# Kernel optimization log

Measured on AMD Instinct MI355X. Metric: run time of the kernel, lower is better.

Reference implementation:

```python
import jax, jax.numpy as jnp
import numpy as np
from jax import lax

DIM = 96
HEADS = 6
H = W = D = 64
EPS = 1e-12  # torch F.normalize default


def setup_inputs() -> dict:
    key = jax.random.key(0)
    k1, k2, k3, k4 = jax.random.split(key, 4)
    x = jax.random.normal(k1, (1, DIM, H, W, D), dtype=jnp.float32)
    # qkv 1x1 conv weight, stored as (3*dim, dim) matrix
    w_qkv = jax.random.normal(k2, (3 * DIM, DIM), dtype=jnp.float32) * (1.0 / np.sqrt(DIM))
    # depthwise 3x3x3 conv weight (OIDHW with I=1, groups=3*dim)
    w_dw = jax.random.normal(k3, (3 * DIM, 1, 3, 3, 3), dtype=jnp.float32) * (1.0 / np.sqrt(27))
    # output 1x1 conv weight as (dim, dim)
    w_proj = jax.random.normal(k4, (DIM, DIM), dtype=jnp.float32) * (1.0 / np.sqrt(DIM))
    temperature = jnp.ones((HEADS, 1, 1), dtype=jnp.float32)
    return {"x": x, "w_qkv": w_qkv, "w_dw": w_dw, "w_proj": w_proj, "temperature": temperature}


def _l2norm(t):
    # torch F.normalize(dim=-1): t / max(||t||, eps)
    n = jnp.sqrt(jnp.sum(t * t, axis=-1, keepdims=True))
    return t / jnp.maximum(n, EPS)


def reference(x, w_qkv, w_dw, w_proj, temperature):
    b, c, h, w, d = x.shape
    ch = c // HEADS  # per-head channels
    # 1x1 conv -> pointwise GEMM over channels
    qkv = jnp.einsum('bchwd,oc->bohwd', x, w_qkv)  # (b, 3c, h, w, d)
    # depthwise 3x3x3 conv, padding 1
    qkv = lax.conv_general_dilated(
        qkv, w_dw, window_strides=(1, 1, 1), padding=[(1, 1)] * 3,
        feature_group_count=3 * c,
        dimension_numbers=('NCDHW', 'OIDHW', 'NCDHW'))
    q, k, v = jnp.split(qkv, 3, axis=1)
    n = h * w * d
    q = q.reshape(b, HEADS, ch, n)
    k = k.reshape(b, HEADS, ch, n)
    v = v.reshape(b, HEADS, ch, n)
    q = _l2norm(q)
    k = _l2norm(k)
    # channel-wise attention: (b, heads, ch, ch)
    attn = jnp.einsum('bhcn,bhdn->bhcd', q, k) * temperature[None]
    attn = jax.nn.softmax(attn, axis=-1)
    out = jnp.einsum('bhcd,bhdn->bhcn', attn, v)  # (b, heads, ch, n)
    out = out.reshape(b, c, h, w, d)
    out = jnp.einsum('bchwd,oc->bohwd', out, w_proj)
    return out
```

## Files before the change

kernel.cpp:

```cpp
#include <hip/hip_runtime.h>
#include <hip/hip_bf16.h>
#include <hip/hip_fp16.h>

#define NTOT 262144
typedef __hip_bfloat16 bf16;
typedef __attribute__((ext_vector_type(4))) float f32x4;
typedef _Float16 f16x8 __attribute__((ext_vector_type(8)));

__device__ inline ushort f2bf(float f){ bf16 b = __float2bfloat16(f); return *(ushort*)&b; }
__device__ inline float bf2f(ushort u){ union{unsigned i;float f;}v; v.i = (unsigned)u<<16; return v.f; }
__device__ inline unsigned h2u(__half2 h){ union{__half2 h; unsigned u;}v; v.h=h; return v.u; }
__device__ inline __half2 u2h(unsigned u){ union{unsigned u; __half2 h;}v; v.u=u; return v.h; }
__device__ inline ushort f2h(float f){ __half h = __float2half_rn(f); return *(ushort*)&h; }

__global__ void detect_dtype(const ushort* __restrict__ w, int* __restrict__ flag) {
  int tid = threadIdx.x;
  int sane = 0;
  for (int i = tid; i < 512; i += 64) {
    ushort u = w[2 * i];
    int e = (u >> 7) & 0xff;
    sane += (e == 0 || (e >= 100 && e <= 140)) ? 1 : 0;
  }
#pragma unroll
  for (int off = 32; off > 0; off >>= 1) sane += __shfl_down(sane, off, 64);
  if (tid == 0) *flag = (sane >= 256) ? 1 : 0;
}

__global__ void cvt_f16(const void* __restrict__ in, ushort* __restrict__ outw,
                        int n, const int* __restrict__ flag) {
  int f = *flag;
  for (int i = blockIdx.x * 256 + threadIdx.x; i < n; i += gridDim.x * 256) {
    float v = f ? bf2f(((const ushort*)in)[i]) : ((const float*)in)[i];
    outw[i] = f2h(v);
  }
}

template<int MODE>
__global__ __launch_bounds__(256)
void transpose96(const void* __restrict__ in, ushort* __restrict__ out,
                 const int* __restrict__ flag) {
  __shared__ float t[96][65];
  const int tid = threadIdx.x;
  const long n0 = (long)blockIdx.x * 64;
  const int f = (MODE == 0) ? *flag : 0;
#pragma unroll
  for (int i = 0; i < 6; i++) {
    int idx = tid + 256 * i;
    int u = idx & 15, c = idx >> 4;
    float v0, v1, v2, v3;
    if (MODE == 0 && !f) {
      float4 q = *(const float4*)((const float*)in + (size_t)c * NTOT + n0 + u * 4);
      v0 = q.x; v1 = q.y; v2 = q.z; v3 = q.w;
    } else if (MODE == 0) {
      uint2 q = *(const uint2*)((const ushort*)in + (size_t)c * NTOT + n0 + u * 4);
      v0 = bf2f((ushort)(q.x & 0xffffu)); v1 = bf2f((ushort)(q.x >> 16));
      v2 = bf2f((ushort)(q.y & 0xffffu)); v3 = bf2f((ushort)(q.y >> 16));
    } else {
      uint2 q = *(const uint2*)((const ushort*)in + (size_t)c * NTOT + n0 + u * 4);
      __half2 a = u2h(q.x), b = u2h(q.y);
      v0 = __half2float(a.x); v1 = __half2float(a.y);
      v2 = __half2float(b.x); v3 = __half2float(b.y);
    }
    t[c][u*4+0] = v0; t[c][u*4+1] = v1; t[c][u*4+2] = v2; t[c][u*4+3] = v3;
  }
  __syncthreads();
#pragma unroll
  for (int i = 0; i < 3; i++) {
    int idx = tid + 256 * i;
    int oq = idx % 12, n = idx / 12;
    unsigned d[4];
#pragma unroll
    for (int j = 0; j < 4; j++) {
      __half2 hp = __floats2half2_rn(t[oq*8 + 2*j][n], t[oq*8 + 2*j + 1][n]);
      d[j] = h2u(hp);
    }
    *(uint4*)(out + (size_t)(n0 + n) * 96 + oq * 8) = make_uint4(d[0], d[1], d[2], d[3]);
  }
}

template<int OF, bool DYNOUT>
__global__ __launch_bounds__(384)
void gemm96f(const ushort* __restrict__ W, const ushort* __restrict__ Xt,
             void* __restrict__ C, const int* __restrict__ flag) {
  const int tid = threadIdx.x;
  const long n0 = (long)blockIdx.x * 64;
  const int wave = tid >> 6, lane = tid & 63;
  const int col = lane & 15, quad = lane >> 4;
  const int f = DYNOUT ? *flag : 0;
  f32x4 acc[OF][4];
#pragma unroll
  for (int a = 0; a < OF; a++)
#pragma unroll
    for (int b = 0; b < 4; b++) acc[a][b] = (f32x4)0.f;
  const int obase = wave * 16 * OF;
#pragma unroll
  for (int ks = 0; ks < 3; ks++) {
    f16x8 bfrag[4];
#pragma unroll
    for (int nf = 0; nf < 4; nf++)
      bfrag[nf] = *(const f16x8*)(Xt + (size_t)(n0 + nf*16 + col) * 96 + ks*32 + quad*8);
#pragma unroll
    for (int of = 0; of < OF; of++) {
      const int o = obase + of*16 + col;
      f16x8 afrag = *(const f16x8*)(W + (size_t)o * 96 + ks*32 + quad*8);
#pragma unroll
      for (int nf = 0; nf < 4; nf++)
        acc[of][nf] = __builtin_amdgcn_mfma_f32_16x16x32_f16(afrag, bfrag[nf], acc[of][nf], 0, 0, 0);
    }
  }
  __shared__ __align__(16) ushort cs[96 * OF][72];
#pragma unroll
  for (int of = 0; of < OF; of++)
#pragma unroll
    for (int nf = 0; nf < 4; nf++)
#pragma unroll
      for (int r = 0; r < 4; r++) {
        int o = obase + of*16 + quad*4 + r;
        cs[o][nf*16 + col] = f2h(acc[of][nf][r]);
      }
  __syncthreads();
  if (!DYNOUT) {
#pragma unroll
    for (int i = 0; i < 2 * OF; i++) {
      int idx = tid + 384 * i;
      int o = idx >> 3, u = idx & 7;
      uint4 v = *(const uint4*)&cs[o][u * 8];
      *(uint4*)((ushort*)C + (size_t)o * NTOT + n0 + u * 8) = v;
    }
  } else {
#pragma unroll
    for (int i = 0; i < 4; i++) {
      int idx = tid + 384 * i;
      int o = idx >> 4, u = idx & 15;
      uint2 v = *(const uint2*)&cs[o][u * 4];
      __half2 a = u2h(v.x), b = u2h(v.y);
      float f0 = __half2float(a.x), f1 = __half2float(a.y);
      float f2 = __half2float(b.x), f3 = __half2float(b.y);
      if (!f) {
        float4 q = {f0, f1, f2, f3};
        *(float4*)((float*)C + (size_t)o * NTOT + n0 + u * 4) = q;
      } else {
        uint2 q = make_uint2(((unsigned)f2bf(f1) << 16) | f2bf(f0),
                             ((unsigned)f2bf(f3) << 16) | f2bf(f2));
        *(uint2*)((ushort*)C + (size_t)o * NTOT + n0 + u * 4) = q;
      }
    }
  }
}

__global__ __launch_bounds__(256)
void dwconv3(const ushort* __restrict__ in, const void* __restrict__ wt,
             ushort* __restrict__ out, const int* __restrict__ flag) {
  const int c = blockIdx.z;
  const int tid = threadIdx.x;
  const int dq = tid & 7;
  const int w = blockIdx.y * 8 + ((tid >> 3) & 7);
  const int h = blockIdx.x * 4 + (tid >> 6);
  const int d0 = dq * 8;
  __shared__ __half2 wsm2[27];
  if (tid < 27) {
    int f = *flag;
    float wv = f ? bf2f(((const ushort*)wt)[c * 27 + tid])
                 : ((const float*)wt)[c * 27 + tid];
    wsm2[tid] = __floats2half2_rn(wv, wv);
  }
  __syncthreads();
  const unsigned maskL = (dq == 0) ? 0xFFFF0000u : 0xFFFFFFFFu;
  const unsigned maskR = (dq == 7) ? 0x0000FFFFu : 0xFFFFFFFFu;
  __half2 a0 = u2h(0), a1 = u2h(0), a2 = u2h(0), a3 = u2h(0);
  const size_t cbase = (size_t)c * NTOT;
#pragma unroll
  for (int dh = -1; dh <= 1; dh++) {
    int hh = h + dh;
    if (hh < 0 || hh > 63) continue;
#pragma unroll
    for (int dw = -1; dw <= 1; dw++) {
      int ww = w + dw;
      bool wok = (ww >= 0 && ww <= 63);
      uint4 u = make_uint4(0u, 0u, 0u, 0u);
      if (wok)
        u = *(const uint4*)(in + cbase + ((size_t)hh * 64 + ww) * 64 + d0);
      unsigned P = (unsigned)__shfl_up((int)u.w, 1, 8);
      unsigned N = (unsigned)__shfl_down((int)u.x, 1, 8);
      unsigned S0 = __builtin_amdgcn_perm(u.x, P,   0x05040302) & maskL;
      unsigned S1 = __builtin_amdgcn_perm(u.y, u.x, 0x05040302);
      unsigned S2 = __builtin_amdgcn_perm(u.z, u.y, 0x05040302);
      unsigned S3 = __builtin_amdgcn_perm(u.w, u.z, 0x05040302);
      unsigned R3 = __builtin_amdgcn_perm(N,   u.w, 0x05040302) & maskR;
      const int wb = (dh + 1) * 9 + (dw + 1) * 3;
      __half2 wL = wsm2[wb], wC = wsm2[wb + 1], wR = wsm2[wb + 2];
      a0 = __hfma2(wL, u2h(S0), a0); a0 = __hfma2(wC, u2h(u.x), a0); a0 = __hfma2(wR, u2h(S1), a0);
      a1 = __hfma2(wL, u2h(S1), a1); a1 = __hfma2(wC, u2h(u.y), a1); a1 = __hfma2(wR, u2h(S2), a1);
      a2 = __hfma2(wL, u2h(S2), a2); a2 = __hfma2(wC, u2h(u.z), a2); a2 = __hfma2(wR, u2h(S3), a2);
      a3 = __hfma2(wL, u2h(S3), a3); a3 = __hfma2(wC, u2h(u.w), a3); a3 = __hfma2(wR, u2h(R3), a3);
    }
  }
  *(uint4*)(out + cbase + ((size_t)h * 64 + w) * 64 + d0) =
      make_uint4(h2u(a0), h2u(a1), h2u(a2), h2u(a3));
}

__global__ __launch_bounds__(256)
void gram16(const ushort* __restrict__ qk, float* __restrict__ G) {
  const int hd = blockIdx.y;
  const int tid = threadIdx.x, wave = tid >> 6, lane = tid & 63;
  const int col = lane & 15, quad = lane >> 4;
  const ushort* qp = qk + (size_t)(hd * 16 + col) * NTOT;
  const ushort* kp = qp + (size_t)96 * NTOT;
  f32x4 aqk = (f32x4)0.f, aqq = (f32x4)0.f, akk = (f32x4)0.f;
  const int nbase = blockIdx.x * 4096 + wave * 32 + quad * 8;
#pragma unroll 4
  for (int it = 0; it < 32; it++) {
    f16x8 qf = *(const f16x8*)(qp + nbase + it * 128);
    f16x8 kf = *(const f16x8*)(kp + nbase + it * 128);
    aqk = __builtin_amdgcn_mfma_f32_16x16x32_f16(qf, kf, aqk, 0, 0, 0);
    aqq = __builtin_amdgcn_mfma_f32_16x16x32_f16(qf, qf, aqq, 0, 0, 0);
    akk = __builtin_amdgcn_mfma_f32_16x16x32_f16(kf, kf, akk, 0, 0, 0);
  }
  __shared__ float red[4][64][12];
#pragma unroll
  for (int r = 0; r < 4; r++) {
    red[wave][lane][r]     = aqk[r];
    red[wave][lane][4 + r] = aqq[r];
    red[wave][lane][8 + r] = akk[r];
  }
  __syncthreads();
  if (wave == 0) {
#pragma unroll
    for (int j = 0; j < 12; j++) {
      float v = red[0][lane][j] + red[1][lane][j] + red[2][lane][j] + red[3][lane][j];
      int sub = j >> 2, r = j & 3;
      atomicAdd(&G[hd * 768 + sub * 256 + (quad * 4 + r) * 16 + col], v);
    }
  }
}

__global__ __launch_bounds__(256)
void attn_mix(const float* __restrict__ G, const void* __restrict__ wp,
              const void* __restrict__ temp, ushort* __restrict__ M,
              const int* __restrict__ flag) {
  __shared__ float As[6][16][16];
  const int tid = threadIdx.x;
  const int f = *flag;
  if (tid < 96) {
    int hd = tid >> 4, c = tid & 15;
    const float* Gh = G + hd * 768;
    float qn = fmaxf(sqrtf(fmaxf(Gh[256 + c * 17], 0.f)), 1e-12f);
    float t = f ? bf2f(((const ushort*)temp)[hd]) : ((const float*)temp)[hd];
    float lg[16];
    float mx = -1e30f;
#pragma unroll
    for (int d = 0; d < 16; d++) {
      float kn = fmaxf(sqrtf(fmaxf(Gh[512 + d * 17], 0.f)), 1e-12f);
      lg[d] = Gh[c * 16 + d] / (qn * kn) * t;
      mx = fmaxf(mx, lg[d]);
    }
    float s = 0.f;
#pragma unroll
    for (int d = 0; d < 16; d++) { lg[d] = __expf(lg[d] - mx); s += lg[d]; }
    float inv = 1.f / s;
#pragma unroll
    for (int d = 0; d < 16; d++) As[hd][c][d] = lg[d] * inv;
  }
  __syncthreads();
  for (int i = 0; i < 36; i++) {
    int idx = tid + 256 * i;
    int o = idx / 96, p = idx - o * 96;
    int hd = p >> 4, d = p & 15;
    float s = 0.f;
#pragma unroll
    for (int cc = 0; cc < 16; cc++) {
      float wv = f ? bf2f(((const ushort*)wp)[o * 96 + hd * 16 + cc])
                   : ((const float*)wp)[o * 96 + hd * 16 + cc];
      s += wv * As[hd][cc][d];
    }
    M[idx] = f2h(s);
  }
}

extern "C" void kernel_launch(void* const* d_in, const int* in_sizes, int n_in,
                              void* d_out, int out_size, void* d_ws, size_t ws_size,
                              hipStream_t stream) {
  const void* x      = d_in[0];
  const void* w_qkv  = d_in[1];
  const void* w_dw   = d_in[2];
  const void* w_proj = d_in[3];
  const void* temp   = d_in[4];

  const size_t szQKV = (size_t)288 * NTOT * 2;
  ushort* B1 = (ushort*)d_ws;
  ushort* B2 = (ushort*)((char*)d_ws + szQKV);
  ushort* Xt = B2;
  ushort* Vt = B1;
  char* tail = (char*)d_ws + 2 * szQKV;
  float*  G    = (float*)tail;
  ushort* M    = (ushort*)(tail + 18432);
  ushort* Wh   = (ushort*)(tail + 36864);
  int*    flag = (int*)(tail + 92160);
  if (ws_size < 2 * szQKV + 92160 + 256) return;

  detect_dtype<<<1, 64, 0, stream>>>((const ushort*)w_qkv, flag);
  cvt_f16<<<32, 256, 0, stream>>>(w_qkv, Wh, 288 * 96, flag);
  hipMemsetAsync(G, 0, 4608 * 4, stream);
  transpose96<0><<<4096, 256, 0, stream>>>(x, Xt, flag);
  gemm96f<3, false><<<4096, 384, 0, stream>>>(Wh, Xt, B1, flag);
  dwconv3<<<dim3(16, 8, 288), 256, 0, stream>>>(B1, w_dw, B2, flag);
  gram16<<<dim3(64, 6), 256, 0, stream>>>(B2, G);
  transpose96<1><<<4096, 256, 0, stream>>>(B2 + (size_t)192 * NTOT, Vt, flag);
  attn_mix<<<1, 256, 0, stream>>>(G, w_proj, temp, M, flag);
  gemm96f<1, true><<<4096, 384, 0, stream>>>(M, Vt, d_out, flag);
}
```

Measured before the change: 444.4 us.

## Register-block depthwise conv over four h rows to reuse loaded input rows

The depthwise 3x3x3 conv kernel now has each thread compute four consecutive h outputs instead of one. It streams six input rows per w offset and feeds each row to every output it touches, with the 27 weights hoisted into registers. This replaces 9 loads and 9 shuffle/perm sets per output with 18 per four outputs, and the grid shrinks fourfold. In exchange it uses more registers, which may lower occupancy, and there are fewer blocks.

```diff
diff --git a/kernel.cpp b/kernel.cpp
--- a/kernel.cpp
+++ b/kernel.cpp
@@ -155,7 +155,7 @@
   const int tid = threadIdx.x;
   const int dq = tid & 7;
   const int w = blockIdx.y * 8 + ((tid >> 3) & 7);
-  const int h = blockIdx.x * 4 + (tid >> 6);
+  const int h0 = blockIdx.x * 16 + (tid >> 6) * 4;
   const int d0 = dq * 8;
   __shared__ __half2 wsm2[27];
   if (tid < 27) {
@@ -165,21 +165,29 @@
     wsm2[tid] = __floats2half2_rn(wv, wv);
   }
   __syncthreads();
+  __half2 wreg[27];
+#pragma unroll
+  for (int i = 0; i < 27; i++) wreg[i] = wsm2[i];
   const unsigned maskL = (dq == 0) ? 0xFFFF0000u : 0xFFFFFFFFu;
   const unsigned maskR = (dq == 7) ? 0x0000FFFFu : 0xFFFFFFFFu;
-  __half2 a0 = u2h(0), a1 = u2h(0), a2 = u2h(0), a3 = u2h(0);
+  __half2 acc[4][4];
+#pragma unroll
+  for (int r = 0; r < 4; r++)
+#pragma unroll
+    for (int j = 0; j < 4; j++) acc[r][j] = u2h(0u);
   const size_t cbase = (size_t)c * NTOT;
 #pragma unroll
-  for (int dh = -1; dh <= 1; dh++) {
-    int hh = h + dh;
-    if (hh < 0 || hh > 63) continue;
-#pragma unroll
-    for (int dw = -1; dw <= 1; dw++) {
-      int ww = w + dw;
-      bool wok = (ww >= 0 && ww <= 63);
+  for (int dw = -1; dw <= 1; dw++) {
+    const int ww = w + dw;
+    const bool wok = (ww >= 0 && ww <= 63);
+    const ushort* rowp = in + cbase + (size_t)ww * 64 + d0;
+#pragma unroll
+    for (int e = -1; e <= 4; e++) {
+      const int hh = h0 + e;
+      if (hh < 0 || hh > 63) continue;
       uint4 u = make_uint4(0u, 0u, 0u, 0u);
       if (wok)
-        u = *(const uint4*)(in + cbase + ((size_t)hh * 64 + ww) * 64 + d0);
+        u = *(const uint4*)(rowp + (size_t)hh * 4096);
       unsigned P = (unsigned)__shfl_up((int)u.w, 1, 8);
       unsigned N = (unsigned)__shfl_down((int)u.x, 1, 8);
       unsigned S0 = __builtin_amdgcn_perm(u.x, P,   0x05040302) & maskL;
@@ -187,16 +195,21 @@
       unsigned S2 = __builtin_amdgcn_perm(u.z, u.y, 0x05040302);
       unsigned S3 = __builtin_amdgcn_perm(u.w, u.z, 0x05040302);
       unsigned R3 = __builtin_amdgcn_perm(N,   u.w, 0x05040302) & maskR;
-      const int wb = (dh + 1) * 9 + (dw + 1) * 3;
-      __half2 wL = wsm2[wb], wC = wsm2[wb + 1], wR = wsm2[wb + 2];
-      a0 = __hfma2(wL, u2h(S0), a0); a0 = __hfma2(wC, u2h(u.x), a0); a0 = __hfma2(wR, u2h(S1), a0);
-      a1 = __hfma2(wL, u2h(S1), a1); a1 = __hfma2(wC, u2h(u.y), a1); a1 = __hfma2(wR, u2h(S2), a1);
-      a2 = __hfma2(wL, u2h(S2), a2); a2 = __hfma2(wC, u2h(u.z), a2); a2 = __hfma2(wR, u2h(S3), a2);
-      a3 = __hfma2(wL, u2h(S3), a3); a3 = __hfma2(wC, u2h(u.w), a3); a3 = __hfma2(wR, u2h(R3), a3);
-    }
-  }
-  *(uint4*)(out + cbase + ((size_t)h * 64 + w) * 64 + d0) =
-      make_uint4(h2u(a0), h2u(a1), h2u(a2), h2u(a3));
+#pragma unroll
+      for (int r = (e - 1 < 0 ? 0 : e - 1); r <= (e + 1 > 3 ? 3 : e + 1); r++) {
+        const int wb = (e - r + 1) * 9 + (dw + 1) * 3;
+        const __half2 wL = wreg[wb], wC = wreg[wb + 1], wR = wreg[wb + 2];
+        acc[r][0] = __hfma2(wL, u2h(S0), acc[r][0]); acc[r][0] = __hfma2(wC, u2h(u.x), acc[r][0]); acc[r][0] = __hfma2(wR, u2h(S1), acc[r][0]);
+        acc[r][1] = __hfma2(wL, u2h(S1), acc[r][1]); acc[r][1] = __hfma2(wC, u2h(u.y), acc[r][1]); acc[r][1] = __hfma2(wR, u2h(S2), acc[r][1]);
+        acc[r][2] = __hfma2(wL, u2h(S2), acc[r][2]); acc[r][2] = __hfma2(wC, u2h(u.z), acc[r][2]); acc[r][2] = __hfma2(wR, u2h(S3), acc[r][2]);
+        acc[r][3] = __hfma2(wL, u2h(S3), acc[r][3]); acc[r][3] = __hfma2(wC, u2h(u.w), acc[r][3]); acc[r][3] = __hfma2(wR, u2h(R3), acc[r][3]);
+      }
+    }
+  }
+#pragma unroll
+  for (int r = 0; r < 4; r++)
+    *(uint4*)(out + cbase + ((size_t)(h0 + r) * 64 + w) * 64 + d0) =
+        make_uint4(h2u(acc[r][0]), h2u(acc[r][1]), h2u(acc[r][2]), h2u(acc[r][3]));
 }
 
 __global__ __launch_bounds__(256)
@@ -303,7 +316,7 @@
   hipMemsetAsync(G, 0, 4608 * 4, stream);
   transpose96<0><<<4096, 256, 0, stream>>>(x, Xt, flag);
   gemm96f<3, false><<<4096, 384, 0, stream>>>(Wh, Xt, B1, flag);
-  dwconv3<<<dim3(16, 8, 288), 256, 0, stream>>>(B1, w_dw, B2, flag);
+  dwconv3<<<dim3(4, 8, 288), 256, 0, stream>>>(B1, w_dw, B2, flag);
   gram16<<<dim3(64, 6), 256, 0, stream>>>(B2, G);
   transpose96<1><<<4096, 256, 0, stream>>>(B2 + (size_t)192 * NTOT, Vt, flag);
   attn_mix<<<1, 256, 0, stream>>>(G, w_proj, temp, M, flag);
```

Result: faster. 433.9 us (-2.4%).

## Rewrite depthwise 3x3x3 conv as MFMA banded matmul over LDS-staged slabs

Applied to the files above, without the earlier changes.

Replaces the packed-half2 FMA depthwise conv with a kernel that stages six h-planes of a channel into swizzled LDS and computes the d-axis 3-tap stencil as banded-weight MFMA 16x16x32 products. Each block handles four output h rows for one channel, reusing the loaded planes across rows. Blocks are numbered so that each channel's blocks share one XCD. Accumulation now happens in fp32 rather than fp16. The cost is building the banded A fragments and extra LDS traffic, in exchange for fewer redundant global loads and higher arithmetic throughput.

```diff
diff --git a/kernel.cpp b/kernel.cpp
--- a/kernel.cpp
+++ b/kernel.cpp
@@ -148,55 +148,101 @@
   }
 }
 
-__global__ __launch_bounds__(256)
-void dwconv3(const ushort* __restrict__ in, const void* __restrict__ wt,
-             ushort* __restrict__ out, const int* __restrict__ flag) {
-  const int c = blockIdx.z;
+#define SLOT 8448
+__global__ __launch_bounds__(512)
+void dwconv3m(const ushort* __restrict__ in, const void* __restrict__ wt,
+              ushort* __restrict__ out, const int* __restrict__ flag) {
+  __shared__ __align__(16) char slab[6 * SLOT];
+  __shared__ float wf[27];
+  const unsigned B = blockIdx.x;
+  const int xcd = B & 7, s = B >> 3;
+  const int c = xcd + 8 * (s >> 4);
+  const int h0 = (s & 15) * 4;
   const int tid = threadIdx.x;
-  const int dq = tid & 7;
-  const int w = blockIdx.y * 8 + ((tid >> 3) & 7);
-  const int h = blockIdx.x * 4 + (tid >> 6);
-  const int d0 = dq * 8;
-  __shared__ __half2 wsm2[27];
+  const int wave = tid >> 6, lane = tid & 63;
+  const int col = lane & 15, quad = lane >> 4;
+  const size_t cbase = (size_t)c * NTOT;
+
   if (tid < 27) {
     int f = *flag;
-    float wv = f ? bf2f(((const ushort*)wt)[c * 27 + tid])
-                 : ((const float*)wt)[c * 27 + tid];
-    wsm2[tid] = __floats2half2_rn(wv, wv);
-  }
-  __syncthreads();
-  const unsigned maskL = (dq == 0) ? 0xFFFF0000u : 0xFFFFFFFFu;
-  const unsigned maskR = (dq == 7) ? 0x0000FFFFu : 0xFFFFFFFFu;
-  __half2 a0 = u2h(0), a1 = u2h(0), a2 = u2h(0), a3 = u2h(0);
-  const size_t cbase = (size_t)c * NTOT;
-#pragma unroll
-  for (int dh = -1; dh <= 1; dh++) {
-    int hh = h + dh;
+    wf[tid] = f ? bf2f(((const ushort*)wt)[c * 27 + tid])
+                : ((const float*)wt)[c * 27 + tid];
+  }
+
+  if (tid < 96) {
+    int e = tid / 16, gi = tid & 15;
+    int wslot = (gi < 8) ? 0 : 65;
+    int L = e * SLOT + wslot * 128 + (gi & 7) * 16;
+    int phys = L ^ (((L >> 7) & 7) << 4);
+    *(uint4*)(slab + phys) = make_uint4(0u, 0u, 0u, 0u);
+  }
+
+  for (int i = tid; i < 6 * 512; i += 512) {
+    int e = i >> 9, ch = i & 511;
+    int hh = h0 - 1 + e;
     if (hh < 0 || hh > 63) continue;
-#pragma unroll
-    for (int dw = -1; dw <= 1; dw++) {
-      int ww = w + dw;
-      bool wok = (ww >= 0 && ww <= 63);
-      uint4 u = make_uint4(0u, 0u, 0u, 0u);
-      if (wok)
-        u = *(const uint4*)(in + cbase + ((size_t)hh * 64 + ww) * 64 + d0);
-      unsigned P = (unsigned)__shfl_up((int)u.w, 1, 8);
-      unsigned N = (unsigned)__shfl_down((int)u.x, 1, 8);
-      unsigned S0 = __builtin_amdgcn_perm(u.x, P,   0x05040302) & maskL;
-      unsigned S1 = __builtin_amdgcn_perm(u.y, u.x, 0x05040302);
-      unsigned S2 = __builtin_amdgcn_perm(u.z, u.y, 0x05040302);
-      unsigned S3 = __builtin_amdgcn_perm(u.w, u.z, 0x05040302);
-      unsigned R3 = __builtin_amdgcn_perm(N,   u.w, 0x05040302) & maskR;
-      const int wb = (dh + 1) * 9 + (dw + 1) * 3;
-      __half2 wL = wsm2[wb], wC = wsm2[wb + 1], wR = wsm2[wb + 2];
-      a0 = __hfma2(wL, u2h(S0), a0); a0 = __hfma2(wC, u2h(u.x), a0); a0 = __hfma2(wR, u2h(S1), a0);
-      a1 = __hfma2(wL, u2h(S1), a1); a1 = __hfma2(wC, u2h(u.y), a1); a1 = __hfma2(wR, u2h(S2), a1);
-      a2 = __hfma2(wL, u2h(S2), a2); a2 = __hfma2(wC, u2h(u.z), a2); a2 = __hfma2(wR, u2h(S3), a2);
-      a3 = __hfma2(wL, u2h(S3), a3); a3 = __hfma2(wC, u2h(u.w), a3); a3 = __hfma2(wR, u2h(R3), a3);
-    }
-  }
-  *(uint4*)(out + cbase + ((size_t)h * 64 + w) * 64 + d0) =
-      make_uint4(h2u(a0), h2u(a1), h2u(a2), h2u(a3));
+    int L = e * SLOT + 128 + ch * 16;
+    int phys = L ^ (((L >> 7) & 7) << 4);
+    uint4 v = *(const uint4*)((const char*)(in + cbase + hh * 4096) + ch * 16);
+    *(uint4*)(slab + phys) = v;
+  }
+  __syncthreads();
+
+  const int w0 = (wave & 3) * 16;
+  const int jthalf = wave >> 2;
+#pragma unroll
+  for (int jj = 0; jj < 2; jj++) {
+    const int jt = jthalf * 2 + jj;
+    const int bi = (jt + 1) >> 1;
+    const int s2 = 32 * jt - 16 * bi;
+    const int off0 = quad * 8 - col - bi * 8;
+    f16x8 af[9];
+#pragma unroll
+    for (int dh1 = 0; dh1 < 3; dh1++)
+#pragma unroll
+      for (int dw1 = 0; dw1 < 3; dw1++) {
+        const float wl = wf[dh1 * 9 + dw1 * 3 + 0];
+        const float wc = wf[dh1 * 9 + dw1 * 3 + 1];
+        const float wr = wf[dh1 * 9 + dw1 * 3 + 2];
+        f16x8 a;
+#pragma unroll
+        for (int j = 0; j < 8; j++) {
+          int t = off0 + j;
+          float v = (t == -1) ? wl : (t == 0) ? wc : (t == 1) ? wr : 0.f;
+          a[j] = (_Float16)v;
+        }
+        af[dh1 * 3 + dw1] = a;
+      }
+    f32x4 acc[4];
+#pragma unroll
+    for (int r = 0; r < 4; r++) acc[r] = (f32x4)0.f;
+#pragma unroll
+    for (int e = 0; e < 6; e++) {
+      int hh = h0 - 1 + e;
+      if (hh < 0 || hh > 63) continue;
+      f16x8 bfr[3];
+#pragma unroll
+      for (int dw = 0; dw < 3; dw++) {
+        int L = e * SLOT + (w0 + col + dw) * 128 + s2 + quad * 16;
+        int phys = L ^ (((L >> 7) & 7) << 4);
+        bfr[dw] = *(const f16x8*)(slab + phys);
+      }
+#pragma unroll
+      for (int r = 0; r < 4; r++) {
+        if (r < e - 2 || r > e) continue;
+        const int dh1 = e - r;
+#pragma unroll
+        for (int dw = 0; dw < 3; dw++)
+          acc[r] = __builtin_amdgcn_mfma_f32_16x16x32_f16(af[dh1 * 3 + dw], bfr[dw], acc[r], 0, 0, 0);
+      }
+    }
+#pragma unroll
+    for (int r = 0; r < 4; r++) {
+      uint2 pv = make_uint2(((unsigned)f2h(acc[r][1]) << 16) | f2h(acc[r][0]),
+                            ((unsigned)f2h(acc[r][3]) << 16) | f2h(acc[r][2]));
+      *(uint2*)(out + cbase + (size_t)((h0 + r) * 64 + w0 + col) * 64 + jt * 16 + quad * 4) = pv;
+    }
+  }
 }
 
 __global__ __launch_bounds__(256)
@@ -303,7 +349,7 @@
   hipMemsetAsync(G, 0, 4608 * 4, stream);
   transpose96<0><<<4096, 256, 0, stream>>>(x, Xt, flag);
   gemm96f<3, false><<<4096, 384, 0, stream>>>(Wh, Xt, B1, flag);
-  dwconv3<<<dim3(16, 8, 288), 256, 0, stream>>>(B1, w_dw, B2, flag);
+  dwconv3m<<<4608, 512, 0, stream>>>(B1, w_dw, B2, flag);
   gram16<<<dim3(64, 6), 256, 0, stream>>>(B2, G);
   transpose96<1><<<4096, 256, 0, stream>>>(B2 + (size_t)192 * NTOT, Vt, flag);
   attn_mix<<<1, 256, 0, stream>>>(G, w_proj, temp, M, flag);
```

New measurement: 556.5 us. 25.2% more time.
